# Performance work log

Measured on AMD Instinct MI355X. Metric: run time of the kernel, lower is better.

The kernel has to match this reference:

```python
import jax, jax.numpy as jnp
import numpy as np

B, S, D, DS, NSLOT = 2, 1024, 1024, 320, 512
H, CH = 4, 5
DFF = 4 * D
MAXIT = 2


def _ln(x, g, b, eps=1e-5):
    m = x.mean(-1, keepdims=True)
    v = ((x - m) ** 2).mean(-1, keepdims=True)
    return (x - m) * jax.lax.rsqrt(v + eps) * g + b


def _mha(x, Wq, Wk, Wv, Wo, bq, bk, bv, bo, nh):
    b_, s_, d_ = x.shape
    hd = d_ // nh
    q = (x @ Wq + bq).reshape(b_, s_, nh, hd)
    k = (x @ Wk + bk).reshape(b_, s_, nh, hd)
    v = (x @ Wv + bv).reshape(b_, s_, nh, hd)
    a = jax.nn.softmax(jnp.einsum('bqhd,bkhd->bhqk', q, k) * (hd ** -0.5), axis=-1)
    o = jnp.einsum('bhqk,bkhd->bqhd', a, v).reshape(b_, s_, d_)
    return o @ Wo + bo


def setup_inputs():
    key = jax.random.key(0)
    ks = iter(jax.random.split(key, 64))
    n = lambda shape: jax.random.normal(next(ks), shape, jnp.float32) * 0.02
    z = lambda shape: jnp.zeros(shape, jnp.float32)
    o = lambda shape: jnp.ones(shape, jnp.float32)
    return dict(
        x=jax.random.normal(next(ks), (B, S, D), jnp.float32),
        cache=jax.random.normal(next(ks), (B, NSLOT, DS), jnp.float32),
        iter_emb=n((16, D)),
        rq_w=n((D, D)), rg_w=n((D, 1)), rg_b=z((1,)), ck_w=n((DS, D)), cv_w=n((DS, D)),
        aq_w=n((D, D)), ak_w=n((D, D)), av_w=n((D, D)), ao_w=n((D, D)),
        aq_b=z((D,)), ak_b=z((D,)), av_b=z((D,)), ao_b=z((D,)),
        f1_w=n((D, DFF)), f1_b=z((DFF,)), f2_w=n((DFF, D)), f2_b=z((D,)),
        n1_g=o((D,)), n1_b=z((D,)), n2_g=o((D,)), n2_b=z((D,)),
        sq_w=n((DS, DS)), tk_w=n((D, DS)), tv_w=n((D, DS)), wg_w=n((D, 1)), wg_b=z((1,)),
        cq_w=n((DS, DS)), ck2_w=n((DS, DS)), cv2_w=n((DS, DS)), co_w=n((DS, DS)),
        cq_b=z((DS,)), ck2_b=z((DS,)), cv2_b=z((DS,)), co_b=z((DS,)),
        cn_g=o((DS,)), cn_b=z((DS,)),
        max_iterations=MAXIT,
    )


def reference(x, cache, iter_emb, rq_w, rg_w, rg_b, ck_w, cv_w,
              aq_w, ak_w, av_w, ao_w, aq_b, ak_b, av_b, ao_b,
              f1_w, f1_b, f2_w, f2_b, n1_g, n1_b, n2_g, n2_b,
              sq_w, tk_w, tv_w, wg_w, wg_b,
              cq_w, ck2_w, cv2_w, co_w, cq_b, ck2_b, cv2_b, co_b, cn_g, cn_b,
              max_iterations):
    def mem_read(h, cc):
        # gather from cache: gated cross-attention readout
        q = h @ rq_w                                   # [B,S,D]
        k = cc @ ck_w                                  # [B,N,D]
        v = cc @ cv_w                                  # [B,N,D]
        a = jax.nn.softmax(jnp.einsum('bsd,bnd->bsn', q, k) * (D ** -0.5), axis=-1)
        readout = jnp.einsum('bsn,bnd->bsd', a, v)
        gate = jax.nn.sigmoid(h @ rg_w + rg_b)          # [B,S,1] soft read gate
        return h + gate * readout

    def compute_block(h):
        # faithful to ComputeBlock (non-linear-attention branch): norm1 used twice
        hn = _ln(h, n1_g, n1_b)
        attn = _mha(hn, aq_w, ak_w, av_w, ao_w, aq_b, ak_b, av_b, ao_b, H)
        h = _ln(h + attn, n1_g, n1_b)
        ffn = jax.nn.gelu(h @ f1_w + f1_b) @ f2_w + f2_b
        return _ln(h + ffn, n2_g, n2_b)

    def mem_write(h, cc):
        # importance-scored scatter: slots attend over tokens, gated by importance
        sq = cc @ sq_w                                  # [B,N,DS]
        tk = h @ tk_w                                   # [B,S,DS]
        tv = h @ tv_w                                   # [B,S,DS]
        gate = jax.nn.sigmoid(h @ wg_w + wg_b)          # [B,S,1] soft write gate
        a = jax.nn.softmax(jnp.einsum('bnd,bsd->bns', sq, tk) * (DS ** -0.5), axis=-1)
        upd = jnp.einsum('bns,bsd->bnd', a, gate * tv)
        return cc + upd

    def cache_self_attn(cc):
        attn = _mha(cc, cq_w, ck2_w, cv2_w, co_w, cq_b, ck2_b, cv2_b, co_b, CH)
        return _ln(cc + attn, cn_g, cn_b)

    h = x
    cc = cache
    layer_input = x
    h_prev = None
    for it in range(max_iterations):
        h = h + iter_emb[it][None, None, :]
        if it > 0:
            h = h + layer_input + h_prev
        h_enh = mem_read(h, cc)
        h_comp = compute_block(h_enh)
        cc = mem_write(h_comp, cc)
        cc = cache_self_attn(cc)
        h = h_comp
        h_prev = jax.lax.stop_gradient(h_comp)  # torch: h_prev = h_computed.detach()
    return h
```

## Files before the change

### kernel.cpp

```cpp
#include <hip/hip_runtime.h>
#include <cstdint>

constexpr int B_ = 2, S_ = 1024, D_ = 1024, DS_ = 320, NSLOT_ = 512;
constexpr int H_ = 4, CH_ = 5, DFF_ = 4096;
constexpr int HD_ = D_ / H_;
constexpr int CHD_ = DS_ / CH_;
constexpr int BS_ = B_ * S_;
constexpr int BNS_ = B_ * NSLOT_;

typedef unsigned short u16;
typedef __attribute__((ext_vector_type(8))) short bf16x8;
typedef __attribute__((ext_vector_type(4))) float f32x4;
typedef __attribute__((ext_vector_type(4))) u16 u16x4;
typedef long long ll;

__device__ __forceinline__ u16 f2bf(float f) {
  unsigned u = __float_as_uint(f);
  return (u16)((u + 0x7FFFu + ((u >> 16) & 1u)) >> 16);
}
__device__ __forceinline__ float bf2f(u16 h) { return __uint_as_float((unsigned)h << 16); }

__device__ __forceinline__ void gload16(const void* g, void* l) {
  __builtin_amdgcn_global_load_lds((const __attribute__((address_space(1))) void*)g,
                                   (__attribute__((address_space(3))) void*)l, 16, 0, 0);
}

template<int BN>
__global__ __launch_bounds__(512, 4)
void k_gemm(const u16* __restrict__ A, int lda, ll sA, ll sA2,
            const u16* __restrict__ Bp, int ldb, ll sB, ll sB2,
            float* __restrict__ outF, u16* __restrict__ outB,
            int ldc, ll sC, ll sC2,
            u16* __restrict__ outBT, int ldt, ll sT, ll sT2,
            int K, int zdiv, const float* __restrict__ bias,
            const float* __restrict__ rowscale, int rscfrom,
            int splitcol, int act)
{
  constexpr int BM = 128;
  constexpr int MI = (BN == 128) ? 2 : 1;
  constexpr int NI = 4;
  constexpr int WROWS = MI * 16;
  constexpr int ABYT = BM * 128;
  constexpr int BBYT = BN * 128;
  constexpr int BUF = ABYT + BBYT;
  const int z = blockIdx.z, zb = z / zdiv, zr = z - zb * zdiv;
  A  += (ll)zb * sA + (ll)zr * sA2;
  Bp += (ll)zb * sB + (ll)zr * sB2;
  const ll cof = (ll)zb * sC + (ll)zr * sC2;
  const ll tof = (ll)zb * sT + (ll)zr * sT2;
  const int bm = blockIdx.y * BM, bn = blockIdx.x * BN;
  __shared__ __align__(16) char lds[2 * BUF];
  const int tid = threadIdx.x;
  const int lane = tid & 63, wid = tid >> 6;
  const int wm = (BN == 128) ? (wid >> 1) : wid;
  const int wn = (BN == 128) ? (wid & 1) : 0;
  const int rowb = wm * WROWS, colb = wn * 64;

  f32x4 acc[MI][NI];
  const f32x4 fz = {0.f, 0.f, 0.f, 0.f};
  #pragma unroll
  for (int i = 0; i < MI; ++i)
    #pragma unroll
    for (int j = 0; j < NI; ++j) acc[i][j] = fz;

  const int trow = tid >> 3;
  const int tg   = ((tid & 7) ^ (trow & 7)) * 8;
  const u16* gA  = A + (ll)(bm + trow) * lda + tg;
  const u16* gA2 = gA + (ll)64 * lda;
  const u16* gB  = Bp + (ll)(bn + trow) * ldb + tg;
  const u16* gB2 = gB + (ll)64 * ldb;

  const int r = lane & 15, q = lane >> 4;
  const int c7 = r & 7;
  const int gs0 = ((q) ^ c7) << 4;
  const int gs1 = ((4 + q) ^ c7) << 4;
  int aoff[MI], boff[NI];
  #pragma unroll
  for (int i = 0; i < MI; ++i) aoff[i] = (rowb + i * 16 + r) * 128;
  #pragma unroll
  for (int j = 0; j < NI; ++j) boff[j] = (colb + j * 16 + r) * 128;

  auto stage = [&](int buf, int it) {
    char* la = lds + buf * BUF + wid * 1024;
    char* lb = la + ABYT;
    const int ko = it << 6;
    gload16(gA + ko, la);
    gload16(gA2 + ko, la + 8192);
    gload16(gB + ko, lb);
    if constexpr (BN == 128) gload16(gB2 + ko, lb + 8192);
  };

  const int nsteps = K >> 6;
  stage(0, 0);
  int bufp = 0;
  for (int it = 0; it < nsteps; ++it) {
    if (it + 1 < nsteps) {
      stage(bufp ^ 1, it + 1);
      if constexpr (BN == 128) asm volatile("s_waitcnt vmcnt(4)" ::: "memory");
      else                     asm volatile("s_waitcnt vmcnt(3)" ::: "memory");
    } else {
      asm volatile("s_waitcnt vmcnt(0)" ::: "memory");
    }
    __builtin_amdgcn_s_barrier();
    __builtin_amdgcn_sched_barrier(0);
    const char* pa = lds + bufp * BUF;
    const char* pb = pa + ABYT;
    #pragma unroll
    for (int s = 0; s < 2; ++s) {
      const int gso = s ? gs1 : gs0;
      bf16x8 af[MI], bv[NI];
      #pragma unroll
      for (int i = 0; i < MI; ++i) af[i] = *(const bf16x8*)(pa + aoff[i] + gso);
      #pragma unroll
      for (int j = 0; j < NI; ++j) bv[j] = *(const bf16x8*)(pb + boff[j] + gso);
      #pragma unroll
      for (int i = 0; i < MI; ++i)
        #pragma unroll
        for (int j = 0; j < NI; ++j)
          acc[i][j] = __builtin_amdgcn_mfma_f32_16x16x32_bf16(af[i], bv[j], acc[i][j], 0, 0, 0);
    }
    asm volatile("s_waitcnt lgkmcnt(0)" ::: "memory");
    __builtin_amdgcn_sched_barrier(0);
    __builtin_amdgcn_s_barrier();
    bufp ^= 1;
  }

  const int fr = lane & 15, fq = lane >> 4;
  #pragma unroll
  for (int i = 0; i < MI; ++i) {
    const int r0 = bm + rowb + i * 16 + fq * 4;
    #pragma unroll
    for (int j = 0; j < NI; ++j) {
      const int cn = bn + colb + j * 16 + fr;
      const float bvv = bias ? bias[cn] : 0.f;
      const bool doRs = rowscale && (cn >= rscfrom);
      float vv[4];
      #pragma unroll
      for (int t = 0; t < 4; ++t) {
        float v = acc[i][j][t] + bvv;
        if (doRs) v *= rowscale[r0 + t];
        if (act) v = 0.5f * v * (1.f + tanhf(0.7978845608028654f * (v + 0.044715f * v * v * v)));
        vv[t] = v;
      }
      if (cn < splitcol) {
        if (outF) {
          #pragma unroll
          for (int t = 0; t < 4; ++t) outF[cof + (ll)(r0 + t) * ldc + cn] = vv[t];
        }
        if (outB) {
          #pragma unroll
          for (int t = 0; t < 4; ++t) outB[cof + (ll)(r0 + t) * ldc + cn] = f2bf(vv[t]);
        }
      } else {
        u16x4 pk = {f2bf(vv[0]), f2bf(vv[1]), f2bf(vv[2]), f2bf(vv[3])};
        *(u16x4*)(outBT + tof + (ll)(cn - splitcol) * ldt + r0) = pk;
      }
    }
  }
}

__global__ __launch_bounds__(256)
void k_tcvt(const float* __restrict__ in, u16* __restrict__ out, int R, int C)
{
  __shared__ float t[32][33];
  const int bx = blockIdx.x * 32, by = blockIdx.y * 32;
  const int tx = threadIdx.x & 31, ty = threadIdx.x >> 5;
  #pragma unroll
  for (int i = 0; i < 32; i += 8)
    t[ty + i][tx] = in[(ll)(by + ty + i) * C + bx + tx];
  __syncthreads();
  #pragma unroll
  for (int i = 0; i < 32; i += 8)
    out[(ll)(bx + ty + i) * R + by + tx] = f2bf(t[tx][ty + i]);
}

__global__ __launch_bounds__(256)
void k_cvt(const float* __restrict__ in, u16* __restrict__ out, int n)
{
  int i = blockIdx.x * 256 + threadIdx.x;
  if (i < n) out[i] = f2bf(in[i]);
}

__global__ __launch_bounds__(256)
void k_cat3f(float* __restrict__ dst, const float* __restrict__ a, int na,
             const float* __restrict__ b, int nb, const float* __restrict__ c, int nc)
{
  int i = blockIdx.x * 256 + threadIdx.x;
  if (i < na) dst[i] = a[i];
  else if (i < na + nb) dst[i] = b[i - na];
  else if (i < na + nb + nc) dst[i] = c[i - na - nb];
}

__global__ __launch_bounds__(256)
void k_softmax_b16(u16* __restrict__ x, int cols, float scale)
{
  u16* p = x + (ll)blockIdx.x * cols;
  const int tid = threadIdx.x;
  __shared__ float red[256];
  float v[4];
  float m = -1e30f;
  #pragma unroll
  for (int i = 0; i < 4; ++i) {
    const int c = tid + (i << 8);
    v[i] = (c < cols) ? bf2f(p[c]) * scale : -1e30f;
    m = fmaxf(m, v[i]);
  }
  red[tid] = m; __syncthreads();
  for (int s = 128; s > 0; s >>= 1) { if (tid < s) red[tid] = fmaxf(red[tid], red[tid + s]); __syncthreads(); }
  m = red[0]; __syncthreads();
  float sum = 0.f;
  #pragma unroll
  for (int i = 0; i < 4; ++i) { v[i] = expf(v[i] - m); sum += v[i]; }
  red[tid] = sum; __syncthreads();
  for (int s = 128; s > 0; s >>= 1) { if (tid < s) red[tid] += red[tid + s]; __syncthreads(); }
  const float inv = 1.f / red[0];
  #pragma unroll
  for (int i = 0; i < 4; ++i) {
    const int c = tid + (i << 8);
    if (c < cols) p[c] = f2bf(v[i] * inv);
  }
}

__global__ __launch_bounds__(256)
void k_layernorm(const float* __restrict__ x, const float* __restrict__ res,
                 const float* __restrict__ res2, const float* __restrict__ rbias,
                 const float* __restrict__ g, const float* __restrict__ b,
                 float* __restrict__ outF, u16* __restrict__ outB, int cols)
{
  const ll ro = (ll)blockIdx.x * cols;
  const float* px = x + ro;
  const float* pr = res ? res + ro : nullptr;
  const float* p2 = res2 ? res2 + ro : nullptr;
  __shared__ float red[256];
  const int tid = threadIdx.x;
  auto val = [&](int c) {
    float v = px[c];
    if (pr) v += pr[c];
    if (p2) v += p2[c];
    if (rbias) v += rbias[c];
    return v;
  };
  float s = 0.f;
  for (int c = tid; c < cols; c += 256) s += val(c);
  red[tid] = s; __syncthreads();
  for (int t = 128; t > 0; t >>= 1) { if (tid < t) red[tid] += red[tid + t]; __syncthreads(); }
  const float mean = red[0] / cols; __syncthreads();
  float s2 = 0.f;
  for (int c = tid; c < cols; c += 256) { float v = val(c) - mean; s2 += v * v; }
  red[tid] = s2; __syncthreads();
  for (int t = 128; t > 0; t >>= 1) { if (tid < t) red[tid] += red[tid + t]; __syncthreads(); }
  const float inv = rsqrtf(red[0] / cols + 1e-5f);
  for (int c = tid; c < cols; c += 256) {
    float v = (val(c) - mean) * inv * g[c] + b[c];
    if (outF) outF[ro + c] = v;
    if (outB) outB[ro + c] = f2bf(v);
  }
}

__global__ __launch_bounds__(256)
void k_gate(const float* __restrict__ x, const float* __restrict__ w,
            const float* __restrict__ b0, float* __restrict__ out, int cols)
{
  const int lane = threadIdx.x & 63;
  const int wv = threadIdx.x >> 6;
  const ll row = (ll)blockIdx.x * 4 + wv;
  const float* p = x + row * cols;
  float s = 0.f;
  for (int c = lane; c < cols; c += 64) s += p[c] * w[c];
  #pragma unroll
  for (int off = 32; off > 0; off >>= 1) s += __shfl_down(s, off);
  if (lane == 0) out[row] = 1.0f / (1.0f + expf(-(s + b0[0])));
}

__global__ __launch_bounds__(256)
void k_combine2(float* __restrict__ oF, u16* __restrict__ oB,
                const float* __restrict__ a, float sa, const float* __restrict__ b,
                const float* __restrict__ emb, int n, int Dm1)
{
  int i = blockIdx.x * 256 + threadIdx.x;
  if (i >= n) return;
  float v = sa * a[i];
  if (b) v += b[i];
  v += emb[i & Dm1];
  oF[i] = v; oB[i] = f2bf(v);
}

__global__ __launch_bounds__(256)
void k_gated_add(float* __restrict__ out, const float* __restrict__ h,
                 const float* __restrict__ r, const float* __restrict__ gate, int n, int Dv)
{
  int i = blockIdx.x * 256 + threadIdx.x;
  if (i >= n) return;
  out[i] = h[i] + gate[i / Dv] * r[i];
}

__global__ __launch_bounds__(256)
void k_add2(float* __restrict__ oF, u16* __restrict__ oB,
            const float* __restrict__ a, const float* __restrict__ b, int n)
{
  int i = blockIdx.x * 256 + threadIdx.x;
  if (i >= n) return;
  float v = a[i] + b[i];
  oF[i] = v; oB[i] = f2bf(v);
}

extern "C" void kernel_launch(void* const* d_in, const int* in_sizes, int n_in,
                              void* d_out, int out_size, void* d_ws, size_t ws_size,
                              hipStream_t stream)
{
  (void)in_sizes; (void)n_in; (void)out_size;
  const float* x        = (const float*)d_in[0];
  const float* cache0   = (const float*)d_in[1];
  const float* iter_emb = (const float*)d_in[2];
  const float* rq_w     = (const float*)d_in[3];
  const float* rg_w     = (const float*)d_in[4];
  const float* rg_b     = (const float*)d_in[5];
  const float* ck_w     = (const float*)d_in[6];
  const float* cv_w     = (const float*)d_in[7];
  const float* aq_w     = (const float*)d_in[8];
  const float* ak_w     = (const float*)d_in[9];
  const float* av_w     = (const float*)d_in[10];
  const float* ao_w     = (const float*)d_in[11];
  const float* aq_b     = (const float*)d_in[12];
  const float* ak_b     = (const float*)d_in[13];
  const float* av_b     = (const float*)d_in[14];
  const float* ao_b     = (const float*)d_in[15];
  const float* f1_w     = (const float*)d_in[16];
  const float* f1_b     = (const float*)d_in[17];
  const float* f2_w     = (const float*)d_in[18];
  const float* f2_b     = (const float*)d_in[19];
  const float* n1_g     = (const float*)d_in[20];
  const float* n1_b     = (const float*)d_in[21];
  const float* n2_g     = (const float*)d_in[22];
  const float* n2_b     = (const float*)d_in[23];
  const float* sq_w     = (const float*)d_in[24];
  const float* tk_w     = (const float*)d_in[25];
  const float* tv_w     = (const float*)d_in[26];
  const float* wg_w     = (const float*)d_in[27];
  const float* wg_b     = (const float*)d_in[28];
  const float* cq_w     = (const float*)d_in[29];
  const float* ck2_w    = (const float*)d_in[30];
  const float* cv2_w    = (const float*)d_in[31];
  const float* co_w     = (const float*)d_in[32];
  const float* cq_b     = (const float*)d_in[33];
  const float* ck2_b    = (const float*)d_in[34];
  const float* cv2_b    = (const float*)d_in[35];
  const float* co_b     = (const float*)d_in[36];
  const float* cn_g     = (const float*)d_in[37];
  const float* cn_b     = (const float*)d_in[38];

  float* out = (float*)d_out;

  size_t off = 0;
  char* base = (char*)d_ws;
  auto allocF = [&](size_t n) { float* p = (float*)(base + off); off += n * 4; off = (off + 255) & ~(size_t)255; return p; };
  auto allocH = [&](size_t n) { u16* p = (u16*)(base + off); off += n * 2; off = (off + 255) & ~(size_t)255; return p; };

  float* hbuf  = allocF((size_t)BS_ * D_);
  float* henh  = allocF((size_t)BS_ * D_);
  float* hcomp = allocF((size_t)BS_ * D_);
  float* h2b   = allocF((size_t)BS_ * D_);
  float* tA    = allocF((size_t)2 * BS_ * D_);
  float* gate  = allocF((size_t)BS_);
  float* ccnf  = allocF((size_t)BNS_ * DS_);
  float* updf  = allocF((size_t)BNS_ * DS_);
  float* coo   = allocF((size_t)BNS_ * DS_);
  float* ccwf  = allocF((size_t)BNS_ * DS_);
  float* qkvb  = allocF(3 * D_);
  float* cqkvb = allocF(3 * DS_);
  u16* rqT  = allocH((size_t)D_ * D_);
  u16* ckT  = allocH((size_t)D_ * DS_);
  u16* cvT  = allocH((size_t)D_ * DS_);
  u16* aqT  = allocH((size_t)D_ * D_);
  u16* akT  = allocH((size_t)D_ * D_);
  u16* avT  = allocH((size_t)D_ * D_);
  u16* aoT  = allocH((size_t)D_ * D_);
  u16* f1T  = allocH((size_t)DFF_ * D_);
  u16* f2T  = allocH((size_t)D_ * DFF_);
  u16* sqT  = allocH((size_t)DS_ * DS_);
  u16* tkT  = allocH((size_t)DS_ * D_);
  u16* tvTw = allocH((size_t)DS_ * D_);
  u16* cqT  = allocH((size_t)DS_ * DS_);
  u16* ck2T = allocH((size_t)DS_ * DS_);
  u16* cv2T = allocH((size_t)DS_ * DS_);
  u16* coT  = allocH((size_t)DS_ * DS_);
  u16* bb1  = allocH((size_t)BS_ * D_);
  u16* bb2  = allocH((size_t)BS_ * D_);
  u16* bb3  = allocH((size_t)BS_ * D_);
  u16* bb4  = allocH((size_t)BS_ * D_);
  u16* bb5  = allocH((size_t)B_ * H_ * S_ * S_);
  u16* bbQK = allocH((size_t)BS_ * 2 * D_);
  u16* bbCQK= allocH((size_t)BNS_ * 2 * DS_);
  u16* cc0b = allocH((size_t)BNS_ * DS_);
  u16* ccwb = allocH((size_t)BNS_ * DS_);
  u16* sqb  = allocH((size_t)BNS_ * DS_);
  u16* tkb  = allocH((size_t)BS_ * DS_);
  u16* tvTb = allocH((size_t)DS_ * BS_);
  u16* ccnb = allocH((size_t)BNS_ * DS_);
  u16* cv2Tb= allocH((size_t)DS_ * BNS_);
  u16* csab = allocH((size_t)BNS_ * DS_);
  if (off > ws_size) return;
  (void)cvT; (void)akT; (void)avT; (void)tvTw; (void)ck2T; (void)cv2T;

  auto gemm = [&](int M, int N, int K, int z, int zdiv,
                  const u16* Ap, int lda, ll sa, ll sa2,
                  const u16* Bq, int ldb, ll sb, ll sb2,
                  float* oF, u16* oB, int ldc, ll sc, ll sc2,
                  u16* oBT, int ldt, ll st, ll st2,
                  const float* bias, const float* rsc, int rscfrom,
                  int splitcol, int act) {
    const ll b64 = (ll)(N / 64) * (M / 128) * z;
    if (N % 128 == 0 && b64 > 768 && (splitcol % 128) == 0) {
      dim3 g(N / 128, M / 128, z);
      k_gemm<128><<<g, 512, 0, stream>>>(Ap, lda, sa, sa2, Bq, ldb, sb, sb2,
          oF, oB, ldc, sc, sc2, oBT, ldt, st, st2, K, zdiv, bias, rsc, rscfrom, splitcol, act);
    } else {
      dim3 g(N / 64, M / 128, z);
      k_gemm<64><<<g, 512, 0, stream>>>(Ap, lda, sa, sa2, Bq, ldb, sb, sb2,
          oF, oB, ldc, sc, sc2, oBT, ldt, st, st2, K, zdiv, bias, rsc, rscfrom, splitcol, act);
    }
  };
  auto tcvt = [&](const float* in, u16* o, int R, int C) {
    dim3 g(C / 32, R / 32);
    k_tcvt<<<g, 256, 0, stream>>>(in, o, R, C);
  };
  auto lnorm = [&](const float* xp, const float* rp, const float* rp2, const float* rb,
                   const float* g, const float* b, float* oF, u16* oB, int rows, int cols) {
    k_layernorm<<<rows, 256, 0, stream>>>(xp, rp, rp2, rb, g, b, oF, oB, cols);
  };
  auto eg = [](int n) { return dim3((n + 255) / 256); };

  tcvt(rq_w, rqT, D_, D_);
  tcvt(ck_w, ckT, DS_, D_);
  tcvt(cv_w, cvT, DS_, D_);
  tcvt(aq_w, aqT, D_, D_);
  tcvt(ak_w, akT, D_, D_);
  tcvt(av_w, avT, D_, D_);
  tcvt(ao_w, aoT, D_, D_);
  tcvt(f1_w, f1T, D_, DFF_);
  tcvt(f2_w, f2T, DFF_, D_);
  tcvt(sq_w, sqT, DS_, DS_);
  tcvt(tk_w, tkT, D_, DS_);
  tcvt(tv_w, tvTw, D_, DS_);
  tcvt(cq_w, cqT, DS_, DS_);
  tcvt(ck2_w, ck2T, DS_, DS_);
  tcvt(cv2_w, cv2T, DS_, DS_);
  tcvt(co_w, coT, DS_, DS_);
  k_cvt<<<eg(BNS_ * DS_), 256, 0, stream>>>(cache0, cc0b, BNS_ * DS_);
  k_cat3f<<<eg(3 * D_), 256, 0, stream>>>(qkvb, aq_b, D_, ak_b, D_, av_b, D_);
  k_cat3f<<<eg(3 * DS_), 256, 0, stream>>>(cqkvb, cq_b, DS_, ck2_b, DS_, cv2_b, DS_);

  auto mem_read = [&](const float* h_f, const u16* h_b, const u16* cc_b, float* o_henh) {
    gemm(BS_, D_, D_, 1, 1, h_b, D_, 0, 0, rqT, D_, 0, 0,
         nullptr, bb2, D_, 0, 0, nullptr, 0, 0, 0,
         nullptr, nullptr, 0, D_, 0);
    gemm(BNS_, 2 * D_, DS_, 1, 1, cc_b, DS_, 0, 0, ckT, DS_, 0, 0,
         nullptr, bb3, D_, 0, 0, bb4, BNS_, 0, 0,
         nullptr, nullptr, 0, D_, 0);
    gemm(S_, NSLOT_, D_, B_, 1, bb2, D_, (ll)S_ * D_, 0,
         bb3, D_, (ll)NSLOT_ * D_, 0,
         nullptr, bb5, NSLOT_, (ll)S_ * NSLOT_, 0, nullptr, 0, 0, 0,
         nullptr, nullptr, 0, NSLOT_, 0);
    k_softmax_b16<<<B_ * S_, 256, 0, stream>>>(bb5, NSLOT_, 0.03125f);
    gemm(S_, D_, NSLOT_, B_, 1, bb5, NSLOT_, (ll)S_ * NSLOT_, 0,
         bb4, BNS_, NSLOT_, 0,
         tA, nullptr, D_, (ll)S_ * D_, 0, nullptr, 0, 0, 0,
         nullptr, nullptr, 0, D_, 0);
    k_gate<<<BS_ / 4, 256, 0, stream>>>(h_f, rg_w, rg_b, gate, D_);
    k_gated_add<<<eg(BS_ * D_), 256, 0, stream>>>(o_henh, h_f, tA, gate, BS_ * D_, D_);
  };

  auto compute_block = [&](const float* he, float* oF, u16* oB) {
    lnorm(he, nullptr, nullptr, nullptr, n1_g, n1_b, nullptr, bb1, BS_, D_);
    gemm(BS_, 3 * D_, D_, 1, 1, bb1, D_, 0, 0, aqT, D_, 0, 0,
         nullptr, bbQK, 2 * D_, 0, 0, bb4, BS_, 0, 0,
         qkvb, nullptr, 0, 2 * D_, 0);
    gemm(S_, S_, HD_, B_ * H_, H_,
         bbQK, 2 * D_, (ll)S_ * 2 * D_, HD_,
         bbQK + D_, 2 * D_, (ll)S_ * 2 * D_, HD_,
         nullptr, bb5, S_, (ll)H_ * S_ * S_, (ll)S_ * S_, nullptr, 0, 0, 0,
         nullptr, nullptr, 0, S_, 0);
    k_softmax_b16<<<B_ * H_ * S_, 256, 0, stream>>>(bb5, S_, 0.0625f);
    gemm(S_, HD_, S_, B_ * H_, H_,
         bb5, S_, (ll)H_ * S_ * S_, (ll)S_ * S_,
         bb4, BS_, S_, (ll)HD_ * BS_,
         nullptr, bb2, D_, (ll)S_ * D_, HD_, nullptr, 0, 0, 0,
         nullptr, nullptr, 0, HD_, 0);
    gemm(BS_, D_, D_, 1, 1, bb2, D_, 0, 0, aoT, D_, 0, 0,
         tA, nullptr, D_, 0, 0, nullptr, 0, 0, 0,
         ao_b, nullptr, 0, D_, 0);
    lnorm(he, tA, nullptr, nullptr, n1_g, n1_b, h2b, bb1, BS_, D_);
    gemm(BS_, DFF_, D_, 1, 1, bb1, D_, 0, 0, f1T, D_, 0, 0,
         nullptr, bb5, DFF_, 0, 0, nullptr, 0, 0, 0,
         f1_b, nullptr, 0, DFF_, 1);
    gemm(BS_, D_, 2048, 2, 2, bb5, DFF_, 0, 2048, f2T, DFF_, 0, 2048,
         tA, nullptr, D_, 0, (ll)BS_ * D_, nullptr, 0, 0, 0,
         nullptr, nullptr, 0, D_, 0);
    lnorm(h2b, tA, tA + (ll)BS_ * D_, f2_b, n2_g, n2_b, oF, oB, BS_, D_);
  };

  auto mem_write_csa = [&](const float* hc_f, const u16* hc_b,
                           const float* ccin_f, const u16* ccin_b) {
    gemm(BNS_, DS_, DS_, 1, 1, ccin_b, DS_, 0, 0, sqT, DS_, 0, 0,
         nullptr, sqb, DS_, 0, 0, nullptr, 0, 0, 0,
         nullptr, nullptr, 0, DS_, 0);
    k_gate<<<BS_ / 4, 256, 0, stream>>>(hc_f, wg_w, wg_b, gate, D_);
    gemm(BS_, 2 * DS_, D_, 1, 1, hc_b, D_, 0, 0, tkT, D_, 0, 0,
         nullptr, tkb, DS_, 0, 0, tvTb, BS_, 0, 0,
         nullptr, gate, DS_, DS_, 0);
    gemm(NSLOT_, S_, DS_, B_, 1, sqb, DS_, (ll)NSLOT_ * DS_, 0,
         tkb, DS_, (ll)S_ * DS_, 0,
         nullptr, bb5, S_, (ll)NSLOT_ * S_, 0, nullptr, 0, 0, 0,
         nullptr, nullptr, 0, S_, 0);
    k_softmax_b16<<<B_ * NSLOT_, 256, 0, stream>>>(bb5, S_, 0.05590169943749474f);
    gemm(NSLOT_, DS_, S_, B_, 1, bb5, S_, (ll)NSLOT_ * S_, 0,
         tvTb, BS_, S_, 0,
         updf, nullptr, DS_, (ll)NSLOT_ * DS_, 0, nullptr, 0, 0, 0,
         nullptr, nullptr, 0, DS_, 0);
    k_add2<<<eg(BNS_ * DS_), 256, 0, stream>>>(ccnf, ccnb, ccin_f, updf, BNS_ * DS_);
    gemm(BNS_, 3 * DS_, DS_, 1, 1, ccnb, DS_, 0, 0, cqT, DS_, 0, 0,
         nullptr, bbCQK, 2 * DS_, 0, 0, cv2Tb, BNS_, 0, 0,
         cqkvb, nullptr, 0, 2 * DS_, 0);
    gemm(NSLOT_, NSLOT_, CHD_, B_ * CH_, CH_,
         bbCQK, 2 * DS_, (ll)NSLOT_ * 2 * DS_, CHD_,
         bbCQK + DS_, 2 * DS_, (ll)NSLOT_ * 2 * DS_, CHD_,
         nullptr, bb5, NSLOT_, (ll)CH_ * NSLOT_ * NSLOT_, (ll)NSLOT_ * NSLOT_,
         nullptr, 0, 0, 0, nullptr, nullptr, 0, NSLOT_, 0);
    k_softmax_b16<<<B_ * CH_ * NSLOT_, 256, 0, stream>>>(bb5, NSLOT_, 0.125f);
    gemm(NSLOT_, CHD_, NSLOT_, B_ * CH_, CH_,
         bb5, NSLOT_, (ll)CH_ * NSLOT_ * NSLOT_, (ll)NSLOT_ * NSLOT_,
         cv2Tb, BNS_, NSLOT_, (ll)CHD_ * BNS_,
         nullptr, csab, DS_, (ll)NSLOT_ * DS_, CHD_, nullptr, 0, 0, 0,
         nullptr, nullptr, 0, CHD_, 0);
    gemm(BNS_, DS_, DS_, 1, 1, csab, DS_, 0, 0, coT, DS_, 0, 0,
         coo, nullptr, DS_, 0, 0, nullptr, 0, 0, 0,
         co_b, nullptr, 0, DS_, 0);
    lnorm(ccnf, coo, nullptr, nullptr, cn_g, cn_b, ccwf, ccwb, BNS_, DS_);
  };

  k_combine2<<<eg(BS_ * D_), 256, 0, stream>>>(hbuf, bb1, x, 1.0f, nullptr, iter_emb, BS_ * D_, D_ - 1);
  mem_read(hbuf, bb1, cc0b, henh);
  compute_block(henh, hcomp, bb3);
  mem_write_csa(hcomp, bb3, cache0, cc0b);

  k_combine2<<<eg(BS_ * D_), 256, 0, stream>>>(hbuf, bb1, hcomp, 2.0f, x, iter_emb + D_, BS_ * D_, D_ - 1);
  mem_read(hbuf, bb1, ccwb, henh);
  compute_block(henh, out, nullptr);
}
```

Measured before the change: 578.3 us.

## Restructure GEMM K-loop sync, batch weight transposes, fuse gate with add

The GEMM main loop now waits for all outstanding loads and issues the next-stage prefetch after the barrier, which drops the trailing barrier per iteration. The sixteen weight transpose-convert launches become one launch driven by a table. The memory-read gate dot product and gated residual add are fused into one per-row kernel. These cut launch overhead and one barrier per step. The cost is weaker load/compute overlap, since each step waits on vmcnt(0) before compute, and there is a possible race: the prefetch into the other buffer is no longer fenced from slow waves still reading that buffer.

```diff
diff --git a/kernel.cpp b/kernel.cpp
--- a/kernel.cpp
+++ b/kernel.cpp
@@ -94,15 +94,10 @@
   stage(0, 0);
   int bufp = 0;
   for (int it = 0; it < nsteps; ++it) {
-    if (it + 1 < nsteps) {
-      stage(bufp ^ 1, it + 1);
-      if constexpr (BN == 128) asm volatile("s_waitcnt vmcnt(4)" ::: "memory");
-      else                     asm volatile("s_waitcnt vmcnt(3)" ::: "memory");
-    } else {
-      asm volatile("s_waitcnt vmcnt(0)" ::: "memory");
-    }
+    asm volatile("s_waitcnt vmcnt(0)" ::: "memory");
     __builtin_amdgcn_s_barrier();
     __builtin_amdgcn_sched_barrier(0);
+    if (it + 1 < nsteps) stage(bufp ^ 1, it + 1);
     const char* pa = lds + bufp * BUF;
     const char* pb = pa + ABYT;
     #pragma unroll
@@ -121,7 +116,6 @@
     }
     asm volatile("s_waitcnt lgkmcnt(0)" ::: "memory");
     __builtin_amdgcn_sched_barrier(0);
-    __builtin_amdgcn_s_barrier();
     bufp ^= 1;
   }
 
@@ -159,11 +153,29 @@
   }
 }
 
-__global__ __launch_bounds__(256)
-void k_tcvt(const float* __restrict__ in, u16* __restrict__ out, int R, int C)
+struct PrepTable {
+  const float* src[16];
+  u16* dst[16];
+  int R[16];
+  int C[16];
+  int off[17];
+};
+
+__global__ __launch_bounds__(256)
+void k_prep_all(PrepTable T)
 {
   __shared__ float t[32][33];
-  const int bx = blockIdx.x * 32, by = blockIdx.y * 32;
+  const int b = blockIdx.x;
+  int w = 0;
+  #pragma unroll
+  for (int i = 1; i < 16; ++i) if (b >= T.off[i]) w = i;
+  const int lb = b - T.off[w];
+  const int tilesC = T.C[w] >> 5;
+  const int by = (lb / tilesC) << 5;
+  const int bx = (lb - (lb / tilesC) * tilesC) << 5;
+  const float* in = T.src[w];
+  u16* out = T.dst[w];
+  const int R = T.R[w], C = T.C[w];
   const int tx = threadIdx.x & 31, ty = threadIdx.x >> 5;
   #pragma unroll
   for (int i = 0; i < 32; i += 8)
@@ -258,6 +270,24 @@
 }
 
 __global__ __launch_bounds__(256)
+void k_gate_add(float* __restrict__ out, const float* __restrict__ h,
+                const float* __restrict__ r, const float* __restrict__ w,
+                const float* __restrict__ b0, int cols)
+{
+  const ll ro = (ll)blockIdx.x * cols;
+  const float* ph = h + ro;
+  const float* pr = r + ro;
+  __shared__ float red[256];
+  const int tid = threadIdx.x;
+  float s = 0.f;
+  for (int c = tid; c < cols; c += 256) s += ph[c] * w[c];
+  red[tid] = s; __syncthreads();
+  for (int t = 128; t > 0; t >>= 1) { if (tid < t) red[tid] += red[tid + t]; __syncthreads(); }
+  const float g = 1.0f / (1.0f + expf(-(red[0] + b0[0])));
+  for (int c = tid; c < cols; c += 256) out[ro + c] = ph[c] + g * pr[c];
+}
+
+__global__ __launch_bounds__(256)
 void k_gate(const float* __restrict__ x, const float* __restrict__ w,
             const float* __restrict__ b0, float* __restrict__ out, int cols)
 {
@@ -283,15 +313,6 @@
   if (b) v += b[i];
   v += emb[i & Dm1];
   oF[i] = v; oB[i] = f2bf(v);
-}
-
-__global__ __launch_bounds__(256)
-void k_gated_add(float* __restrict__ out, const float* __restrict__ h,
-                 const float* __restrict__ r, const float* __restrict__ gate, int n, int Dv)
-{
-  int i = blockIdx.x * 256 + threadIdx.x;
-  if (i >= n) return;
-  out[i] = h[i] + gate[i / Dv] * r[i];
 }
 
 __global__ __launch_bounds__(256)
@@ -420,32 +441,29 @@
           oF, oB, ldc, sc, sc2, oBT, ldt, st, st2, K, zdiv, bias, rsc, rscfrom, splitcol, act);
     }
   };
-  auto tcvt = [&](const float* in, u16* o, int R, int C) {
-    dim3 g(C / 32, R / 32);
-    k_tcvt<<<g, 256, 0, stream>>>(in, o, R, C);
-  };
   auto lnorm = [&](const float* xp, const float* rp, const float* rp2, const float* rb,
                    const float* g, const float* b, float* oF, u16* oB, int rows, int cols) {
     k_layernorm<<<rows, 256, 0, stream>>>(xp, rp, rp2, rb, g, b, oF, oB, cols);
   };
   auto eg = [](int n) { return dim3((n + 255) / 256); };
 
-  tcvt(rq_w, rqT, D_, D_);
-  tcvt(ck_w, ckT, DS_, D_);
-  tcvt(cv_w, cvT, DS_, D_);
-  tcvt(aq_w, aqT, D_, D_);
-  tcvt(ak_w, akT, D_, D_);
-  tcvt(av_w, avT, D_, D_);
-  tcvt(ao_w, aoT, D_, D_);
-  tcvt(f1_w, f1T, D_, DFF_);
-  tcvt(f2_w, f2T, DFF_, D_);
-  tcvt(sq_w, sqT, DS_, DS_);
-  tcvt(tk_w, tkT, D_, DS_);
-  tcvt(tv_w, tvTw, D_, DS_);
-  tcvt(cq_w, cqT, DS_, DS_);
-  tcvt(ck2_w, ck2T, DS_, DS_);
-  tcvt(cv2_w, cv2T, DS_, DS_);
-  tcvt(co_w, coT, DS_, DS_);
+  {
+    PrepTable T;
+    const float* srcs[16] = {rq_w, ck_w, cv_w, aq_w, ak_w, av_w, ao_w, f1_w,
+                             f2_w, sq_w, tk_w, tv_w, cq_w, ck2_w, cv2_w, co_w};
+    u16* dsts[16] = {rqT, ckT, cvT, aqT, akT, avT, aoT, f1T,
+                     f2T, sqT, tkT, tvTw, cqT, ck2T, cv2T, coT};
+    const int Rs[16] = {D_, DS_, DS_, D_, D_, D_, D_, D_, DFF_, DS_, D_, D_, DS_, DS_, DS_, DS_};
+    const int Cs[16] = {D_, D_, D_, D_, D_, D_, D_, DFF_, D_, DS_, DS_, DS_, DS_, DS_, DS_, DS_};
+    int acc0 = 0;
+    for (int i = 0; i < 16; ++i) {
+      T.src[i] = srcs[i]; T.dst[i] = dsts[i]; T.R[i] = Rs[i]; T.C[i] = Cs[i];
+      T.off[i] = acc0;
+      acc0 += (Rs[i] >> 5) * (Cs[i] >> 5);
+    }
+    T.off[16] = acc0;
+    k_prep_all<<<acc0, 256, 0, stream>>>(T);
+  }
   k_cvt<<<eg(BNS_ * DS_), 256, 0, stream>>>(cache0, cc0b, BNS_ * DS_);
   k_cat3f<<<eg(3 * D_), 256, 0, stream>>>(qkvb, aq_b, D_, ak_b, D_, av_b, D_);
   k_cat3f<<<eg(3 * DS_), 256, 0, stream>>>(cqkvb, cq_b, DS_, ck2_b, DS_, cv2_b, DS_);
@@ -466,8 +484,7 @@
          bb4, BNS_, NSLOT_, 0,
          tA, nullptr, D_, (ll)S_ * D_, 0, nullptr, 0, 0, 0,
          nullptr, nullptr, 0, D_, 0);
-    k_gate<<<BS_ / 4, 256, 0, stream>>>(h_f, rg_w, rg_b, gate, D_);
-    k_gated_add<<<eg(BS_ * D_), 256, 0, stream>>>(o_henh, h_f, tA, gate, BS_ * D_, D_);
+    k_gate_add<<<BS_, 256, 0, stream>>>(o_henh, h_f, tA, rg_w, rg_b, D_);
   };
 
   auto compute_block = [&](const float* he, float* oF, u16* oB) {
```

Result: faster. 553.0 us (-4.4%).
